# Kernel optimization log

Measured on AMD Instinct MI355X. Metric: run time of the kernel, lower is better.

Reference implementation:

```python
import jax, jax.numpy as jnp
import numpy as np

NUM_SAMPLES = 8192   # num_parallel_samples
HIDDEN = 512
EMB = 40             # embedding_dim(10) * freq_map['H'](4)
C_IN = 1
TIME_FEAT = 4
HIST_LEN = 336
PRED_LEN = 48
MIN_SCALE = 1e-5
SAMPLE_KEY_SEED = 42


def _gru_cell(h, x, W_ih, W_hh, b_ih, b_hh):
    # torch GRU cell: gates stacked as [r, z, n] along rows of W (each HIDDEN)
    gi = x @ W_ih.T + b_ih            # [B, 3H]
    gh = h @ W_hh.T + b_hh            # [B, 3H]
    H = h.shape[-1]
    i_r, i_z, i_n = gi[:, :H], gi[:, H:2 * H], gi[:, 2 * H:]
    h_r, h_z, h_n = gh[:, :H], gh[:, H:2 * H], gh[:, 2 * H:]
    r = jax.nn.sigmoid(i_r + h_r)
    z = jax.nn.sigmoid(i_z + h_z)
    n = jnp.tanh(i_n + r * h_n)
    return (1.0 - z) * n + z * h


def setup_inputs() -> dict:
    key = jax.random.key(0)
    ks = jax.random.split(key, 16)
    f32 = jnp.float32
    inp = {
        "x": jax.random.normal(ks[0], (1, HIST_LEN, C_IN), dtype=f32),
        "x_mark": jax.random.normal(ks[1], (1, HIST_LEN, TIME_FEAT), dtype=f32),
        "y_mark": jax.random.normal(ks[2], (1, PRED_LEN, TIME_FEAT), dtype=f32),
        "mode": 0,
        # time_feat_embedding: Linear(4 -> 40), torch layout [out, in]
        "W_emb": jax.random.normal(ks[3], (EMB, TIME_FEAT), dtype=f32) * 0.05,
        "b_emb": jnp.zeros((EMB,), dtype=f32),
        # GRU (1 layer): input size = c_in + EMB = 41
        "W_ih": jax.random.normal(ks[4], (3 * HIDDEN, C_IN + EMB), dtype=f32) * 0.05,
        "W_hh": jax.random.normal(ks[5], (3 * HIDDEN, HIDDEN), dtype=f32) * 0.05,
        "b_ih": jnp.zeros((3 * HIDDEN,), dtype=f32),
        "b_hh": jnp.zeros((3 * HIDDEN,), dtype=f32),
        # StudentT args projection: three Linear(HIDDEN -> 1)
        "W_df": jax.random.normal(ks[6], (1, HIDDEN), dtype=f32) * 0.05,
        "b_df": jnp.zeros((1,), dtype=f32),
        "W_loc": jax.random.normal(ks[7], (1, HIDDEN), dtype=f32) * 0.05,
        "b_loc": jnp.zeros((1,), dtype=f32),
        "W_sc": jax.random.normal(ks[8], (1, HIDDEN), dtype=f32) * 0.05,
        "b_sc": jnp.zeros((1,), dtype=f32),
    }
    return inp


def _deepar_sample(x, x_mark, y_mark, W_emb, b_emb, W_ih, W_hh, b_ih, b_hh,
                   W_df, b_df, W_loc, b_loc, W_sc, b_sc):
    S = NUM_SAMPLES
    # ---- encoder (unroll_encoder with y=None) ----
    scale = jnp.clip(jnp.mean(jnp.abs(x), axis=1, keepdims=True), MIN_SCALE, None)  # [1,1,1]
    seq = x / scale
    tfe = x_mark @ W_emb.T + b_emb                      # [1, T, EMB]
    enc_in = jnp.concatenate([seq, tfe], axis=-1)       # [1, T, 41]
    h0 = jnp.zeros((1, HIDDEN), dtype=x.dtype)

    def enc_step(h, xt):  # xt: [1, 41]
        h = _gru_cell(h, xt, W_ih, W_hh, b_ih, b_hh)
        return h, None

    h_T, _ = jax.lax.scan(enc_step, h0, jnp.swapaxes(enc_in, 0, 1))  # [1, H]

    # ---- sampling decoder ----
    h = jnp.broadcast_to(h_T, (S, HIDDEN))              # repeat state across samples
    # note: original feeds the UNSCALED last observation as first decoder input
    tgt0 = jnp.broadcast_to(x[0, -1, :], (S, C_IN))     # [S, 1]
    emb_y = y_mark[0] @ W_emb.T + b_emb                 # [pred_len, EMB]
    scale_s = scale[0, 0, 0]                            # scalar (batch=1, c=1)
    base_key = jax.random.key(SAMPLE_KEY_SEED)

    def dec_step(carry, xs):
        h, tgt = carry
        e_k, k = xs
        inp = jnp.concatenate([tgt, jnp.broadcast_to(e_k, (S, EMB))], axis=-1)  # [S, 41]
        h = _gru_cell(h, inp, W_ih, W_hh, b_ih, b_hh)
        # StudentTOutput domain map: df = 2 + softplus, loc raw, scale = softplus
        df = 2.0 + jax.nn.softplus(h @ W_df.T + b_df)   # [S, 1]
        loc = h @ W_loc.T + b_loc                       # [S, 1]
        sc = jax.nn.softplus(h @ W_sc.T + b_sc)         # [S, 1]
        eps = jax.random.t(jax.random.fold_in(base_key, k),
                           jax.lax.stop_gradient(df), df.shape, dtype=df.dtype)
        sample = (loc + sc * eps) * scale_s             # AffineTransformed(scale)
        return (h, sample), sample

    ks = jnp.arange(PRED_LEN)
    _, samples = jax.lax.scan(dec_step, (h, tgt0), (emb_y, ks))  # [pred_len, S, 1]
    return jnp.transpose(samples, (1, 0, 2))            # [S, pred_len, c_out]


def reference(x, x_mark, y_mark, mode, W_emb, b_emb, W_ih, W_hh, b_ih, b_hh,
              W_df, b_df, W_loc, b_loc, W_sc, b_sc):
    # mode=0 -> sampling/inference path (the kernel target)
    return _deepar_sample(x, x_mark, y_mark, W_emb, b_emb, W_ih, W_hh, b_ih, b_hh,
                          W_df, b_df, W_loc, b_loc, W_sc, b_sc)
```

## Files before the change

kernel.cpp:

```cpp
#include <hip/hip_runtime.h>
#include <cmath>


#define JAX_PARTITIONABLE 1

#define HIDDEN 512
#define EMB 40
#define HIST 336
#define PRED 48
#define S_N 8192
#define ENC_BLOCKS 48

#define HPLANE (8192 * 512)
#define WPLANE (1536 * 512)
#define INV4096 (1.0f / 4096.0f)

typedef __attribute__((ext_vector_type(8))) _Float16 half8;
typedef __attribute__((ext_vector_type(4))) float f32x4;

struct KeyPair { unsigned a, b; };

__device__ __forceinline__ unsigned rotl32_(unsigned v, unsigned s) {
  return (v << s) | (v >> (32u - s));
}

__device__ __forceinline__ KeyPair tf2x32(KeyPair k, unsigned x0, unsigned x1) {
  unsigned ks0 = k.a, ks1 = k.b, ks2 = ks0 ^ ks1 ^ 0x1BD11BDAu;
  x0 += ks0; x1 += ks1;
#define TF_R(r) { x0 += x1; x1 = rotl32_(x1, r); x1 ^= x0; }
  TF_R(13u) TF_R(15u) TF_R(26u) TF_R(6u)  x0 += ks1; x1 += ks2 + 1u;
  TF_R(17u) TF_R(29u) TF_R(16u) TF_R(24u) x0 += ks2; x1 += ks0 + 2u;
  TF_R(13u) TF_R(15u) TF_R(26u) TF_R(6u)  x0 += ks0; x1 += ks1 + 3u;
  TF_R(17u) TF_R(29u) TF_R(16u) TF_R(24u) x0 += ks1; x1 += ks2 + 4u;
  TF_R(13u) TF_R(15u) TF_R(26u) TF_R(6u)  x0 += ks2; x1 += ks0 + 5u;
#undef TF_R
  KeyPair r; r.a = x0; r.b = x1; return r;
}

__device__ __forceinline__ void split2_(KeyPair key, KeyPair& r0, KeyPair& r1) {
#if JAX_PARTITIONABLE
  r0 = tf2x32(key, 0u, 0u);
  r1 = tf2x32(key, 0u, 1u);
#else
  KeyPair p0 = tf2x32(key, 0u, 2u);
  KeyPair p1 = tf2x32(key, 1u, 3u);
  r0.a = p0.a; r0.b = p1.a;
  r1.a = p0.b; r1.b = p1.b;
#endif
}

__device__ __forceinline__ void split3_(KeyPair key, KeyPair& r0, KeyPair& r1, KeyPair& r2) {
#if JAX_PARTITIONABLE
  r0 = tf2x32(key, 0u, 0u);
  r1 = tf2x32(key, 0u, 1u);
  r2 = tf2x32(key, 0u, 2u);
#else
  KeyPair p0 = tf2x32(key, 0u, 3u);
  KeyPair p1 = tf2x32(key, 1u, 4u);
  KeyPair p2 = tf2x32(key, 2u, 5u);
  r0.a = p0.a; r0.b = p1.a;
  r1.a = p2.a; r1.b = p0.b;
  r2.a = p1.b; r2.b = p2.b;
#endif
}

__device__ __forceinline__ unsigned scalar_bits_(KeyPair key) {
#if JAX_PARTITIONABLE
  KeyPair p = tf2x32(key, 0u, 0u);
  return p.a ^ p.b;
#else
  return tf2x32(key, 0u, 0u).a;
#endif
}

__device__ __forceinline__ unsigned batch_bits_8192_(KeyPair key, int s) {
#if JAX_PARTITIONABLE
  KeyPair p = tf2x32(key, 0u, (unsigned)s);
  return p.a ^ p.b;
#else
  if (s < 4096) return tf2x32(key, (unsigned)s, (unsigned)(4096 + s)).a;
  return tf2x32(key, (unsigned)(s - 4096), (unsigned)s).b;
#endif
}

__device__ __forceinline__ KeyPair subkey_of_8192_(KeyPair key, int s) {
#if JAX_PARTITIONABLE
  return tf2x32(key, 0u, (unsigned)s);
#else
  KeyPair r;
  if (s < 4096) {
    r.a = tf2x32(key, (unsigned)(2 * s),     (unsigned)(8192 + 2 * s)).a;
    r.b = tf2x32(key, (unsigned)(2 * s + 1), (unsigned)(8192 + 2 * s + 1)).a;
  } else {
    int m = 2 * s - 8192;
    r.a = tf2x32(key, (unsigned)m,       (unsigned)(m + 8192)).b;
    r.b = tf2x32(key, (unsigned)(m + 1), (unsigned)(m + 1 + 8192)).b;
  }
  return r;
#endif
}

__device__ __forceinline__ float acc_logf_(float x) {
  return (float)log((double)x);
}
__device__ __forceinline__ float acc_expf_(float x) {
  return (float)exp((double)x);
}

__device__ __forceinline__ float bits_to_uniform01_(unsigned bits) {
  return __uint_as_float((bits >> 9) | 0x3F800000u) - 1.0f;
}

__device__ __forceinline__ float xla_log1pf_(float t) {
  #pragma clang fp contract(off)
  float small_ = (1.0f + (-0.5f) * t) * t;
  float large_ = acc_logf_(t + 1.0f);
  return (fabsf(t) < 1e-4f) ? small_ : large_;
}

__device__ float xla_erfinv_(float x) {
  #pragma clang fp contract(off)
  float w = -xla_log1pf_(-(x * x));
  float p;
  if (w < 5.0f) {
    float ww = w - 2.5f;
    p = 2.81022636e-08f;
    p = 3.43273939e-07f + p * ww;
    p = -3.5233877e-06f + p * ww;
    p = -4.39150654e-06f + p * ww;
    p = 0.00021858087f + p * ww;
    p = -0.00125372503f + p * ww;
    p = -0.00417768164f + p * ww;
    p = 0.246640727f + p * ww;
    p = 1.50140941f + p * ww;
  } else {
    float ww = sqrtf(w) - 3.0f;
    p = -0.000200214257f;
    p = 0.000100950558f + p * ww;
    p = 0.00134934322f + p * ww;
    p = -0.00367342844f + p * ww;
    p = 0.00573950773f + p * ww;
    p = -0.0076224613f + p * ww;
    p = 0.00943887047f + p * ww;
    p = 1.00167406f + p * ww;
    p = 2.83297682f + p * ww;
  }
  return p * x;
}

__device__ float bits_to_normal_(unsigned bits) {
  #pragma clang fp contract(off)
  const float lo = __uint_as_float(0xBF7FFFFFu);
  float f = bits_to_uniform01_(bits);
  float u = f * 2.0f + lo;
  u = fmaxf(lo, u);
  return __uint_as_float(0x3FB504F3u) * xla_erfinv_(u);
}

__device__ __forceinline__ float softplus_(float x) {
  #pragma clang fp contract(off)
  float amax = fmaxf(x, 0.0f);
  float e = acc_expf_(-fabsf(x));
  return amax + xla_log1pf_(e);
}

__device__ __forceinline__ float sigmoid_(float v) { return 1.0f / (1.0f + expf(-v)); }

__device__ __forceinline__ unsigned short f2h_(float f) {
  _Float16 h = (_Float16)f;
  return __builtin_bit_cast(unsigned short, h);
}
__device__ __forceinline__ float h2f_(unsigned short b) {
  return (float)__builtin_bit_cast(_Float16, b);
}

__device__ float gamma_sample_(KeyPair gkey, float alpha) {
  #pragma clang fp contract(off)
  const float third = 0.33333334f;
  float d = alpha - third;
  float c = third / sqrtf(d);
  KeyPair key, boost_sub;
  split2_(gkey, key, boost_sub);
  (void)boost_sub;
  float X = 0.0f, V = 1.0f, U = 2.0f;
  for (int guard = 0; guard < 1024; guard++) {
    float X2 = X * X;
    float sq = 1.0f - 0.0331f * (X2 * X2);
    bool cont = false;
    if (U >= sq) {
      float lhs = acc_logf_(U);
      float rhs = (X * 0.5f) + (d * ((1.0f - V) + acc_logf_(V)));
      cont = (lhs >= rhs);
    }
    if (!cont) break;
    KeyPair nkey, xkey, Ukey;
    split3_(key, nkey, xkey, Ukey);
    key = nkey;
    float x, v;
    KeyPair kk = xkey;
    do {
      KeyPair knew, sub;
      split2_(kk, knew, sub);
      kk = knew;
      x = bits_to_normal_(scalar_bits_(sub));
      v = 1.0f + x * c;
    } while (v <= 0.0f);
    X = x * x;
    V = (v * v) * v;
    U = bits_to_uniform01_(scalar_bits_(Ukey));
  }
  return d * V;
}

__device__ float sample_t_eps_(int k, int s, float df) {
  #pragma clang fp contract(off)
  KeyPair base; base.a = 0u; base.b = 42u;
  KeyPair tkey = tf2x32(base, 0u, (unsigned)k);
  KeyPair key_n, key_g;
  split2_(tkey, key_n, key_g);
  float n = bits_to_normal_(batch_bits_8192_(key_n, s));
  KeyPair gkey = subkey_of_8192_(key_g, s);
  float half_df = df * 0.5f;
  float g = gamma_sample_(gkey, half_df);
  return n * sqrtf(half_df / g);
}


__global__ __launch_bounds__(256) void prep_kernel(
    const float* __restrict__ x, const float* __restrict__ x_mark,
    const float* __restrict__ y_mark, const float* __restrict__ W_emb,
    const float* __restrict__ b_emb, float* __restrict__ scale_p,
    float* __restrict__ tfe, float* __restrict__ emb_y,
    unsigned* __restrict__ flags) {
  int tid = threadIdx.x;
  if (tid == 0) {
    float s = 0.0f;
    for (int t = 0; t < HIST; t++) s += fabsf(x[t]);
    float m = s / 336.0f;
    scale_p[0] = fmaxf(m, 1e-5f);
  }
  for (int i = tid; i < ENC_BLOCKS * 16; i += 256) flags[i] = 0u;
  for (int idx = tid; idx < HIST * EMB; idx += 256) {
    int t = idx / EMB, e = idx % EMB;
    float a = b_emb[e];
    for (int f = 0; f < 4; f++) a += x_mark[t * 4 + f] * W_emb[e * 4 + f];
    tfe[idx] = a;
  }
  for (int idx = tid; idx < PRED * EMB; idx += 256) {
    int kk = idx / EMB, e = idx % EMB;
    float a = b_emb[e];
    for (int f = 0; f < 4; f++) a += y_mark[kk * 4 + f] * W_emb[e * 4 + f];
    emb_y[idx] = a;
  }
}

__global__ __launch_bounds__(256) void enc_gi_kernel(
    const float* __restrict__ x, const float* __restrict__ tfe,
    const float* __restrict__ W_ih, const float* __restrict__ b_ih,
    const float* __restrict__ scale_p, float* __restrict__ enc_gi) {
  __shared__ float fe[EMB];
  __shared__ float xs_s;
  int t = blockIdx.x;
  int tid = threadIdx.x;
  if (tid < EMB) fe[tid] = tfe[t * EMB + tid];
  if (tid == 0) xs_s = x[t] / scale_p[0];
  __syncthreads();
  float xs = xs_s;
  for (int r = tid; r < 3 * HIDDEN; r += 256) {
    const float* wr = W_ih + (size_t)r * 41;
    float a = b_ih[r] + wr[0] * xs;
    #pragma unroll
    for (int e = 0; e < EMB; e++) a += wr[1 + e] * fe[e];
    enc_gi[(size_t)t * 1536 + r] = a;
  }
}

__global__ __launch_bounds__(256) void giy_kernel(
    const float* __restrict__ emb_y, const float* __restrict__ W_ih,
    const float* __restrict__ b_ih, float* __restrict__ giy) {
  __shared__ float fe[EMB];
  int k = blockIdx.x;
  int tid = threadIdx.x;
  if (tid < EMB) fe[tid] = emb_y[k * EMB + tid];
  __syncthreads();
  for (int r = tid; r < 3 * HIDDEN; r += 256) {
    const float* wr = W_ih + (size_t)r * 41;
    float a = b_ih[r];
    #pragma unroll
    for (int e = 0; e < EMB; e++) a += wr[1 + e] * fe[e];
    giy[(size_t)k * 1536 + r] = a;
  }
}

__global__ __launch_bounds__(256) void wsplit_kernel(
    const float* __restrict__ W_hh, unsigned short* __restrict__ Wr) {
  int row = blockIdx.x;
  int g = row >> 9;
  int jg = row & 511;
  int jb = jg >> 5, jl = jg & 31;
  size_t dst = ((size_t)jb * 96 + g * 32 + jl) * 512;
  for (int k = threadIdx.x; k < 512; k += 256) {
    float w = W_hh[(size_t)row * 512 + k];
    unsigned short g0 = f2h_(w);
    float r1 = (w - h2f_(g0)) * 4096.0f;
    unsigned short g1 = f2h_(r1);
    Wr[dst + k] = g0;
    Wr[WPLANE + dst + k] = g1;
  }
}

__global__ __launch_bounds__(256) void hsplit_kernel(
    const float* __restrict__ h_T, unsigned short* __restrict__ sT) {
  int i = threadIdx.x;
  for (int j = i; j < 512; j += 256) {
    float v = h_T[j];
    unsigned short f0 = f2h_(v);
    float r1 = (v - h2f_(f0)) * 4096.0f;
    sT[j] = f0;
    sT[512 + j] = f2h_(r1);
  }
}

__global__ __launch_bounds__(128) void h2bcast_kernel(
    const unsigned short* __restrict__ sT, unsigned short* __restrict__ h2) {
  int row = blockIdx.x;
  int tid = threadIdx.x;
  int sp = tid >> 6, c = tid & 63;
  ((uint4*)(h2 + (size_t)sp * HPLANE + (size_t)row * 512))[c] =
      ((const uint4*)(sT + sp * 512))[c];
}

__global__ __launch_bounds__(256) void enc_gru_kernel(
    const float* __restrict__ enc_gi, const float* __restrict__ W_hh,
    const float* __restrict__ b_hh, float* __restrict__ ghbuf,
    unsigned* __restrict__ flags, float* __restrict__ h_T) {
  __shared__ __align__(16) float hs[HIDDEN];
  int tid = threadIdx.x;
  int gtid = blockIdx.x * 256 + tid;
  int row = gtid >> 3;
  int sub = gtid & 7;

  float w[64];
  const float* wp = W_hh + (size_t)row * HIDDEN + sub * 64;
  #pragma unroll
  for (int i = 0; i < 16; i++) {
    float4 v = *(const float4*)(wp + 4 * i);
    w[4 * i + 0] = v.x; w[4 * i + 1] = v.y; w[4 * i + 2] = v.z; w[4 * i + 3] = v.w;
  }
  if (tid < 128) *(float4*)&hs[tid * 4] = make_float4(0.f, 0.f, 0.f, 0.f);
  float bhr0 = b_hh[tid],       bhz0 = b_hh[512 + tid],  bhn0 = b_hh[1024 + tid];
  float bhr1 = b_hh[256 + tid], bhz1 = b_hh[768 + tid],  bhn1 = b_hh[1280 + tid];
  __syncthreads();

  for (int t = 0; t < HIST; t++) {
    float p = 0.0f;
    const float4* hv = (const float4*)&hs[sub * 64];
    #pragma unroll
    for (int i = 0; i < 16; i++) {
      float4 v = hv[i];
      p += w[4 * i + 0] * v.x + w[4 * i + 1] * v.y +
           w[4 * i + 2] * v.z + w[4 * i + 3] * v.w;
    }
    p += __shfl_xor(p, 1, 64);
    p += __shfl_xor(p, 2, 64);
    p += __shfl_xor(p, 4, 64);
    int par = t & 1;
    if (sub == 0)
      __hip_atomic_store(&ghbuf[par * 1536 + row], p, __ATOMIC_RELAXED,
                         __HIP_MEMORY_SCOPE_AGENT);
    __syncthreads();
    if (tid == 0)
      __hip_atomic_store(&flags[blockIdx.x * 16], (unsigned)(t + 1),
                         __ATOMIC_RELEASE, __HIP_MEMORY_SCOPE_AGENT);
    if (tid < ENC_BLOCKS) {
      while (__hip_atomic_load(&flags[tid * 16], __ATOMIC_ACQUIRE,
                               __HIP_MEMORY_SCOPE_AGENT) < (unsigned)(t + 1))
        __builtin_amdgcn_s_sleep(1);
    }
    __syncthreads();
    float hn0, hn1;
    {
      int j = tid;
      float ghr = __hip_atomic_load(&ghbuf[par * 1536 + j], __ATOMIC_RELAXED, __HIP_MEMORY_SCOPE_AGENT);
      float ghz = __hip_atomic_load(&ghbuf[par * 1536 + 512 + j], __ATOMIC_RELAXED, __HIP_MEMORY_SCOPE_AGENT);
      float ghn = __hip_atomic_load(&ghbuf[par * 1536 + 1024 + j], __ATOMIC_RELAXED, __HIP_MEMORY_SCOPE_AGENT);
      float gir = enc_gi[(size_t)t * 1536 + j];
      float giz = enc_gi[(size_t)t * 1536 + 512 + j];
      float gin = enc_gi[(size_t)t * 1536 + 1024 + j];
      float r = sigmoid_(gir + (ghr + bhr0));
      float z = sigmoid_(giz + (ghz + bhz0));
      float n = tanhf(gin + r * (ghn + bhn0));
      hn0 = (1.0f - z) * n + z * hs[j];
    }
    {
      int j = tid + 256;
      float ghr = __hip_atomic_load(&ghbuf[par * 1536 + j], __ATOMIC_RELAXED, __HIP_MEMORY_SCOPE_AGENT);
      float ghz = __hip_atomic_load(&ghbuf[par * 1536 + 512 + j], __ATOMIC_RELAXED, __HIP_MEMORY_SCOPE_AGENT);
      float ghn = __hip_atomic_load(&ghbuf[par * 1536 + 1024 + j], __ATOMIC_RELAXED, __HIP_MEMORY_SCOPE_AGENT);
      float gir = enc_gi[(size_t)t * 1536 + j];
      float giz = enc_gi[(size_t)t * 1536 + 512 + j];
      float gin = enc_gi[(size_t)t * 1536 + 1024 + j];
      float r = sigmoid_(gir + (ghr + bhr1));
      float z = sigmoid_(giz + (ghz + bhz1));
      float n = tanhf(gin + r * (ghn + bhn1));
      hn1 = (1.0f - z) * n + z * hs[j];
    }
    hs[tid] = hn0;
    hs[tid + 256] = hn1;
    __syncthreads();
  }
  if (blockIdx.x == 0 && tid < 128)
    *(float4*)&h_T[tid * 4] = *(float4*)&hs[tid * 4];
}

__global__ __launch_bounds__(256, 2) void dec_gru_mfma(
    const unsigned short* __restrict__ h2_in,
    const unsigned short* __restrict__ Wr,
    const float* __restrict__ giy_k, const float* __restrict__ b_hh,
    const float* __restrict__ W_ih, const float* __restrict__ tgt,
    int tgt_is_x, unsigned short* __restrict__ h2_out,
    const float* __restrict__ W_df, const float* __restrict__ W_loc,
    const float* __restrict__ W_sc, float* __restrict__ partials) {
  __shared__ unsigned short As[2][2][128][32];
  int b_ = blockIdx.x;
  int xcd = b_ & 7, slot = b_ >> 3;
  int mb = xcd * 8 + (slot & 7);
  int jb = slot >> 3;
  int tid = threadIdx.x;
  int lane = tid & 63;
  int wave = tid >> 6;
  int wm = wave >> 1, wn = wave & 1;
  int s0 = mb * 128;
  int q = lane >> 4, c = lane & 15;

  f32x4 accm[4][3], accc[4][3];
  #pragma unroll
  for (int i = 0; i < 4; i++)
    #pragma unroll
    for (int g = 0; g < 3; g++) {
      accm[i][g] = (f32x4){0.f, 0.f, 0.f, 0.f};
      accc[i][g] = (f32x4){0.f, 0.f, 0.f, 0.f};
    }

  float hold[4][4];
  #pragma unroll
  for (int i = 0; i < 4; i++)
    #pragma unroll
    for (int r = 0; r < 4; r++) hold[i][r] = 0.f;

  int asp[4], arow[4], acol[4];
  #pragma unroll
  for (int r = 0; r < 4; r++) {
    int a = r * 256 + tid;
    asp[r] = a >> 9;
    int rem = a & 511;
    arow[r] = rem >> 2;
    acol[r] = rem & 3;
  }

  const unsigned short* Bbase =
      Wr + ((size_t)jb * 96 + wn * 16 + c) * 512 + q * 8;

  #pragma unroll
  for (int r = 0; r < 4; r++) {
    uint4 v = *(const uint4*)(h2_in + (size_t)asp[r] * HPLANE +
                              (size_t)(s0 + arow[r]) * 512 + acol[r] * 8);
    *(uint4*)&As[0][asp[r]][arow[r]][(acol[r] ^ (arow[r] & 3)) * 8] = v;
  }
  half8 Bcur[3][2];
  #pragma unroll
  for (int g = 0; g < 3; g++) {
    Bcur[g][0] = *(const half8*)(Bbase + (size_t)g * 32 * 512);
    Bcur[g][1] = *(const half8*)(Bbase + WPLANE + (size_t)g * 32 * 512);
  }
  __syncthreads();

  int cur = 0;
  for (int kbi = 0; kbi < 16; kbi++) {
    int kb = kbi * 32;
    uint4 Areg[4];
    half8 Bn[3][2];
    if (kbi < 15) {
      #pragma unroll
      for (int r = 0; r < 4; r++)
        Areg[r] = *(const uint4*)(h2_in + (size_t)asp[r] * HPLANE +
                                  (size_t)(s0 + arow[r]) * 512 + kb + 32 +
                                  acol[r] * 8);
      #pragma unroll
      for (int g = 0; g < 3; g++) {
        Bn[g][0] = *(const half8*)(Bbase + (size_t)g * 32 * 512 + kb + 32);
        Bn[g][1] = *(const half8*)(Bbase + WPLANE + (size_t)g * 32 * 512 + kb + 32);
      }
    }
    if (kbi == jb) {
      int cc = wn * 16 + c;
      #pragma unroll
      for (int i = 0; i < 4; i++)
        #pragma unroll
        for (int reg = 0; reg < 4; reg++) {
          int m = wm * 64 + i * 16 + q * 4 + reg;
          int idx = (((cc >> 3) ^ (m & 3)) << 3) + (cc & 7);
          hold[i][reg] = h2f_(As[cur][0][m][idx]) +
                         h2f_(As[cur][1][m][idx]) * INV4096;
        }
    }
    #pragma unroll
    for (int i = 0; i < 4; i++) {
      int m = wm * 64 + i * 16 + c;
      half8 a0 = *(const half8*)&As[cur][0][m][(q ^ (c & 3)) * 8];
      half8 a1 = *(const half8*)&As[cur][1][m][(q ^ (c & 3)) * 8];
      #pragma unroll
      for (int g = 0; g < 3; g++) {
        accm[i][g] = __builtin_amdgcn_mfma_f32_16x16x32_f16(a0, Bcur[g][0], accm[i][g], 0, 0, 0);
        accc[i][g] = __builtin_amdgcn_mfma_f32_16x16x32_f16(a0, Bcur[g][1], accc[i][g], 0, 0, 0);
        accc[i][g] = __builtin_amdgcn_mfma_f32_16x16x32_f16(a1, Bcur[g][0], accc[i][g], 0, 0, 0);
      }
    }
    if (kbi < 15) {
      #pragma unroll
      for (int r = 0; r < 4; r++)
        *(uint4*)&As[cur ^ 1][asp[r]][arow[r]][(acol[r] ^ (arow[r] & 3)) * 8] =
            Areg[r];
      #pragma unroll
      for (int g = 0; g < 3; g++) {
        Bcur[g][0] = Bn[g][0];
        Bcur[g][1] = Bn[g][1];
      }
    }
    __syncthreads();
    cur ^= 1;
  }

  float* pb = (float*)&As[0][0][0][0];
  {
    int j = jb * 32 + wn * 16 + c;
    float gyr = giy_k[j], gyz = giy_k[512 + j], gyn = giy_k[1024 + j];
    float w0r = W_ih[(size_t)j * 41];
    float w0z = W_ih[(size_t)(512 + j) * 41];
    float w0n = W_ih[(size_t)(1024 + j) * 41];
    float bhr = b_hh[j], bhz = b_hh[512 + j], bhn = b_hh[1024 + j];
    float wdj = W_df[j], wlj = W_loc[j], wsj = W_sc[j];
    #pragma unroll
    for (int i = 0; i < 4; i++) {
      #pragma unroll
      for (int reg = 0; reg < 4; reg++) {
        int s = s0 + wm * 64 + i * 16 + q * 4 + reg;
        float tg = tgt_is_x ? tgt[HIST - 1] : tgt[s];
        size_t off = (size_t)s * 512 + j;
        float h_old = hold[i][reg];
        float ghr = accm[i][0][reg] + accc[i][0][reg] * INV4096;
        float ghz = accm[i][1][reg] + accc[i][1][reg] * INV4096;
        float ghn = accm[i][2][reg] + accc[i][2][reg] * INV4096;
        float gr = (gyr + w0r * tg) + (ghr + bhr);
        float gz = (gyz + w0z * tg) + (ghz + bhz);
        float gn_i = gyn + w0n * tg;
        float gn_h = ghn + bhn;
        float r_ = sigmoid_(gr);
        float z_ = sigmoid_(gz);
        float n_ = tanhf(gn_i + r_ * gn_h);
        float hn = (1.0f - z_) * n_ + z_ * h_old;
        unsigned short f0 = f2h_(hn);
        float r1 = (hn - h2f_(f0)) * 4096.0f;
        __builtin_nontemporal_store(f0, &h2_out[off]);
        __builtin_nontemporal_store(f2h_(r1), &h2_out[HPLANE + off]);
        float vd = hn * wdj, vl = hn * wlj, vs = hn * wsj;
        #pragma unroll
        for (int o = 1; o < 16; o <<= 1) {
          vd += __shfl_xor(vd, o, 64);
          vl += __shfl_xor(vl, o, 64);
          vs += __shfl_xor(vs, o, 64);
        }
        if (c == 0) {
          int sl = i * 16 + q * 4 + reg;
          int bix = ((wm * 2 + wn) * 64 + sl) * 3;
          pb[bix + 0] = vd; pb[bix + 1] = vl; pb[bix + 2] = vs;
        }
      }
    }
  }
  __syncthreads();
  if (tid < 128) {
    int wmh = tid >> 6, sl = tid & 63;
    int ia = (wmh * 2 + 0) * 192 + sl * 3;
    int ib = ia + 192;
    int s = s0 + wmh * 64 + sl;
    size_t pofs = (size_t)s * 48 + jb * 3;
    partials[pofs + 0] = pb[ia + 0] + pb[ib + 0];
    partials[pofs + 1] = pb[ia + 1] + pb[ib + 1];
    partials[pofs + 2] = pb[ia + 2] + pb[ib + 2];
  }
}

__global__ __launch_bounds__(64) void dec_head_kernel(
    const float* __restrict__ partials, const float* __restrict__ b_df,
    const float* __restrict__ b_loc, const float* __restrict__ b_sc,
    const float* __restrict__ scale_p, float* __restrict__ tgt,
    float* __restrict__ out, int k) {
  #pragma clang fp contract(off)
  int s = blockIdx.x * 64 + threadIdx.x;
  const float* p = partials + (size_t)s * 48;
  float adf = 0.f, alo = 0.f, asc = 0.f;
  #pragma unroll
  for (int jb = 0; jb < 16; jb++) {
    adf += p[jb * 3 + 0];
    alo += p[jb * 3 + 1];
    asc += p[jb * 3 + 2];
  }
  float df = 2.0f + softplus_(adf + b_df[0]);
  float loc = alo + b_loc[0];
  float sc = softplus_(asc + b_sc[0]);
  float eps = sample_t_eps_(k, s, df);
  float smp = (loc + sc * eps) * scale_p[0];
  out[(size_t)s * PRED + k] = smp;
  tgt[s] = smp;
}

extern "C" void kernel_launch(void* const* d_in, const int* in_sizes, int n_in,
                              void* d_out, int out_size, void* d_ws, size_t ws_size,
                              hipStream_t stream) {
  const float* x      = (const float*)d_in[0];
  const float* x_mark = (const float*)d_in[1];
  const float* y_mark = (const float*)d_in[2];
  const float* W_emb  = (const float*)d_in[4];
  const float* b_emb  = (const float*)d_in[5];
  const float* W_ih   = (const float*)d_in[6];
  const float* W_hh   = (const float*)d_in[7];
  const float* b_ih   = (const float*)d_in[8];
  const float* b_hh   = (const float*)d_in[9];
  const float* W_df   = (const float*)d_in[10];
  const float* b_df   = (const float*)d_in[11];
  const float* W_loc  = (const float*)d_in[12];
  const float* b_loc  = (const float*)d_in[13];
  const float* W_sc   = (const float*)d_in[14];
  const float* b_sc   = (const float*)d_in[15];
  float* out = (float*)d_out;

  float* w = (float*)d_ws;
  unsigned short* h2_a = (unsigned short*)(w);
  unsigned short* h2_b = (unsigned short*)(w + 4194304);
  unsigned short* Wr   = (unsigned short*)(w + 8388608);
  float* enc_gi = w + 9175040;
  float* giy    = w + 9691136;
  float* tfe    = w + 9764864;
  float* emb_y  = w + 9778304;
  float* ghbuf  = w + 9780224;
  float* h_T    = w + 9783296;
  unsigned short* sT = (unsigned short*)(w + 9783808);
  float* tgt    = w + 9784320;
  float* scale_p = w + 9792512;
  unsigned* flags = (unsigned*)(w + 9792516);
  float* partials = w + 9793540;

  prep_kernel<<<1, 256, 0, stream>>>(x, x_mark, y_mark, W_emb, b_emb,
                                     scale_p, tfe, emb_y, flags);
  enc_gi_kernel<<<HIST, 256, 0, stream>>>(x, tfe, W_ih, b_ih, scale_p, enc_gi);
  giy_kernel<<<PRED, 256, 0, stream>>>(emb_y, W_ih, b_ih, giy);
  wsplit_kernel<<<1536, 256, 0, stream>>>(W_hh, Wr);
  enc_gru_kernel<<<ENC_BLOCKS, 256, 0, stream>>>(enc_gi, W_hh, b_hh, ghbuf,
                                                 flags, h_T);
  hsplit_kernel<<<1, 256, 0, stream>>>(h_T, sT);
  h2bcast_kernel<<<S_N, 128, 0, stream>>>(sT, h2_a);

  for (int k = 0; k < PRED; k++) {
    const unsigned short* h_in = (k % 2 == 0) ? h2_a : h2_b;
    unsigned short* h_o = (k % 2 == 0) ? h2_b : h2_a;
    dec_gru_mfma<<<1024, 256, 0, stream>>>(
        h_in, Wr, giy + (size_t)k * 1536, b_hh, W_ih,
        (k == 0) ? x : tgt, (k == 0) ? 1 : 0, h_o,
        W_df, W_loc, W_sc, partials);
    dec_head_kernel<<<S_N / 64, 64, 0, stream>>>(
        partials, b_df, b_loc, b_sc, scale_p, tgt, out, k);
  }
}
```

Baseline: 5.618 ms.

## Replace encoder flag barrier with tagged 64-bit values and double-buffered hidden state

The encoder GRU grid barrier (per-block release flags, an acquire spin by 48 threads, and two __syncthreads) is replaced by packing each gate dot-product with a step tag into a 64-bit word. Every thread spins directly on the six values it needs until their tags match. The hidden state in shared memory is double-buffered so one __syncthreads per step is enough, and the enc_gi loads are hoisted ahead of the dot product to hide their latency. The cost is more global polling traffic from all threads, and correctness relies on the 64-bit stores and loads being atomic.

```diff
diff --git a/kernel.cpp b/kernel.cpp
--- a/kernel.cpp
+++ b/kernel.cpp
@@ -231,7 +231,7 @@
     const float* __restrict__ y_mark, const float* __restrict__ W_emb,
     const float* __restrict__ b_emb, float* __restrict__ scale_p,
     float* __restrict__ tfe, float* __restrict__ emb_y,
-    unsigned* __restrict__ flags) {
+    unsigned long long* __restrict__ gh2) {
   int tid = threadIdx.x;
   if (tid == 0) {
     float s = 0.0f;
@@ -239,7 +239,7 @@
     float m = s / 336.0f;
     scale_p[0] = fmaxf(m, 1e-5f);
   }
-  for (int i = tid; i < ENC_BLOCKS * 16; i += 256) flags[i] = 0u;
+  for (int i = tid; i < 2 * 1536; i += 256) gh2[i] = 0ull;
   for (int idx = tid; idx < HIST * EMB; idx += 256) {
     int t = idx / EMB, e = idx % EMB;
     float a = b_emb[e];
@@ -332,9 +332,9 @@
 
 __global__ __launch_bounds__(256) void enc_gru_kernel(
     const float* __restrict__ enc_gi, const float* __restrict__ W_hh,
-    const float* __restrict__ b_hh, float* __restrict__ ghbuf,
-    unsigned* __restrict__ flags, float* __restrict__ h_T) {
-  __shared__ __align__(16) float hs[HIDDEN];
+    const float* __restrict__ b_hh, unsigned long long* __restrict__ gh2,
+    float* __restrict__ h_T) {
+  __shared__ __align__(16) float hsb[2][HIDDEN];
   int tid = threadIdx.x;
   int gtid = blockIdx.x * 256 + tid;
   int row = gtid >> 3;
@@ -347,14 +347,23 @@
     float4 v = *(const float4*)(wp + 4 * i);
     w[4 * i + 0] = v.x; w[4 * i + 1] = v.y; w[4 * i + 2] = v.z; w[4 * i + 3] = v.w;
   }
-  if (tid < 128) *(float4*)&hs[tid * 4] = make_float4(0.f, 0.f, 0.f, 0.f);
+  if (tid < 128) *(float4*)&hsb[0][tid * 4] = make_float4(0.f, 0.f, 0.f, 0.f);
   float bhr0 = b_hh[tid],       bhz0 = b_hh[512 + tid],  bhn0 = b_hh[1024 + tid];
   float bhr1 = b_hh[256 + tid], bhz1 = b_hh[768 + tid],  bhn1 = b_hh[1280 + tid];
   __syncthreads();
 
   for (int t = 0; t < HIST; t++) {
+    int par = t & 1;
+    unsigned tag = (unsigned)(t + 1);
+    const float* hc = hsb[par];
+    float* hw = hsb[par ^ 1];
+
+    const float* gi = enc_gi + (size_t)t * 1536;
+    float gir0 = gi[tid],        giz0 = gi[512 + tid],  gin0 = gi[1024 + tid];
+    float gir1 = gi[256 + tid],  giz1 = gi[768 + tid],  gin1 = gi[1280 + tid];
+
     float p = 0.0f;
-    const float4* hv = (const float4*)&hs[sub * 64];
+    const float4* hv = (const float4*)&hc[sub * 64];
     #pragma unroll
     for (int i = 0; i < 16; i++) {
       float4 v = hv[i];
@@ -364,53 +373,51 @@
     p += __shfl_xor(p, 1, 64);
     p += __shfl_xor(p, 2, 64);
     p += __shfl_xor(p, 4, 64);
-    int par = t & 1;
-    if (sub == 0)
-      __hip_atomic_store(&ghbuf[par * 1536 + row], p, __ATOMIC_RELAXED,
+    if (sub == 0) {
+      unsigned long long pk =
+          ((unsigned long long)tag << 32) | (unsigned long long)__float_as_uint(p);
+      __hip_atomic_store(&gh2[par * 1536 + row], pk, __ATOMIC_RELAXED,
                          __HIP_MEMORY_SCOPE_AGENT);
+    }
+
+    const unsigned long long* g = gh2 + par * 1536;
+    unsigned long long v0, v1, v2, v3, v4, v5;
+    for (;;) {
+      v0 = __hip_atomic_load(&g[tid],         __ATOMIC_RELAXED, __HIP_MEMORY_SCOPE_AGENT);
+      v1 = __hip_atomic_load(&g[512 + tid],   __ATOMIC_RELAXED, __HIP_MEMORY_SCOPE_AGENT);
+      v2 = __hip_atomic_load(&g[1024 + tid],  __ATOMIC_RELAXED, __HIP_MEMORY_SCOPE_AGENT);
+      v3 = __hip_atomic_load(&g[256 + tid],   __ATOMIC_RELAXED, __HIP_MEMORY_SCOPE_AGENT);
+      v4 = __hip_atomic_load(&g[768 + tid],   __ATOMIC_RELAXED, __HIP_MEMORY_SCOPE_AGENT);
+      v5 = __hip_atomic_load(&g[1280 + tid],  __ATOMIC_RELAXED, __HIP_MEMORY_SCOPE_AGENT);
+      if ((unsigned)(v0 >> 32) == tag && (unsigned)(v1 >> 32) == tag &&
+          (unsigned)(v2 >> 32) == tag && (unsigned)(v3 >> 32) == tag &&
+          (unsigned)(v4 >> 32) == tag && (unsigned)(v5 >> 32) == tag)
+        break;
+      __builtin_amdgcn_s_sleep(1);
+    }
+
+    {
+      float ghr = __uint_as_float((unsigned)v0);
+      float ghz = __uint_as_float((unsigned)v1);
+      float ghn = __uint_as_float((unsigned)v2);
+      float r = sigmoid_(gir0 + (ghr + bhr0));
+      float z = sigmoid_(giz0 + (ghz + bhz0));
+      float n = tanhf(gin0 + r * (ghn + bhn0));
+      hw[tid] = (1.0f - z) * n + z * hc[tid];
+    }
+    {
+      float ghr = __uint_as_float((unsigned)v3);
+      float ghz = __uint_as_float((unsigned)v4);
+      float ghn = __uint_as_float((unsigned)v5);
+      float r = sigmoid_(gir1 + (ghr + bhr1));
+      float z = sigmoid_(giz1 + (ghz + bhz1));
+      float n = tanhf(gin1 + r * (ghn + bhn1));
+      hw[tid + 256] = (1.0f - z) * n + z * hc[tid + 256];
+    }
     __syncthreads();
-    if (tid == 0)
-      __hip_atomic_store(&flags[blockIdx.x * 16], (unsigned)(t + 1),
-                         __ATOMIC_RELEASE, __HIP_MEMORY_SCOPE_AGENT);
-    if (tid < ENC_BLOCKS) {
-      while (__hip_atomic_load(&flags[tid * 16], __ATOMIC_ACQUIRE,
-                               __HIP_MEMORY_SCOPE_AGENT) < (unsigned)(t + 1))
-        __builtin_amdgcn_s_sleep(1);
-    }
-    __syncthreads();
-    float hn0, hn1;
-    {
-      int j = tid;
-      float ghr = __hip_atomic_load(&ghbuf[par * 1536 + j], __ATOMIC_RELAXED, __HIP_MEMORY_SCOPE_AGENT);
-      float ghz = __hip_atomic_load(&ghbuf[par * 1536 + 512 + j], __ATOMIC_RELAXED, __HIP_MEMORY_SCOPE_AGENT);
-      float ghn = __hip_atomic_load(&ghbuf[par * 1536 + 1024 + j], __ATOMIC_RELAXED, __HIP_MEMORY_SCOPE_AGENT);
-      float gir = enc_gi[(size_t)t * 1536 + j];
-      float giz = enc_gi[(size_t)t * 1536 + 512 + j];
-      float gin = enc_gi[(size_t)t * 1536 + 1024 + j];
-      float r = sigmoid_(gir + (ghr + bhr0));
-      float z = sigmoid_(giz + (ghz + bhz0));
-      float n = tanhf(gin + r * (ghn + bhn0));
-      hn0 = (1.0f - z) * n + z * hs[j];
-    }
-    {
-      int j = tid + 256;
-      float ghr = __hip_atomic_load(&ghbuf[par * 1536 + j], __ATOMIC_RELAXED, __HIP_MEMORY_SCOPE_AGENT);
-      float ghz = __hip_atomic_load(&ghbuf[par * 1536 + 512 + j], __ATOMIC_RELAXED, __HIP_MEMORY_SCOPE_AGENT);
-      float ghn = __hip_atomic_load(&ghbuf[par * 1536 + 1024 + j], __ATOMIC_RELAXED, __HIP_MEMORY_SCOPE_AGENT);
-      float gir = enc_gi[(size_t)t * 1536 + j];
-      float giz = enc_gi[(size_t)t * 1536 + 512 + j];
-      float gin = enc_gi[(size_t)t * 1536 + 1024 + j];
-      float r = sigmoid_(gir + (ghr + bhr1));
-      float z = sigmoid_(giz + (ghz + bhz1));
-      float n = tanhf(gin + r * (ghn + bhn1));
-      hn1 = (1.0f - z) * n + z * hs[j];
-    }
-    hs[tid] = hn0;
-    hs[tid + 256] = hn1;
-    __syncthreads();
   }
   if (blockIdx.x == 0 && tid < 128)
-    *(float4*)&h_T[tid * 4] = *(float4*)&hs[tid * 4];
+    *(float4*)&h_T[tid * 4] = *(float4*)&hsb[0][tid * 4];
 }
 
 __global__ __launch_bounds__(256, 2) void dec_gru_mfma(
@@ -643,21 +650,19 @@
   float* giy    = w + 9691136;
   float* tfe    = w + 9764864;
   float* emb_y  = w + 9778304;
-  float* ghbuf  = w + 9780224;
-  float* h_T    = w + 9783296;
-  unsigned short* sT = (unsigned short*)(w + 9783808);
-  float* tgt    = w + 9784320;
-  float* scale_p = w + 9792512;
-  unsigned* flags = (unsigned*)(w + 9792516);
-  float* partials = w + 9793540;
+  unsigned long long* gh2 = (unsigned long long*)(w + 9780224);
+  float* h_T    = w + 9786368;
+  unsigned short* sT = (unsigned short*)(w + 9786880);
+  float* tgt    = w + 9787392;
+  float* scale_p = w + 9795584;
+  float* partials = w + 9795588;
 
   prep_kernel<<<1, 256, 0, stream>>>(x, x_mark, y_mark, W_emb, b_emb,
-                                     scale_p, tfe, emb_y, flags);
+                                     scale_p, tfe, emb_y, gh2);
   enc_gi_kernel<<<HIST, 256, 0, stream>>>(x, tfe, W_ih, b_ih, scale_p, enc_gi);
   giy_kernel<<<PRED, 256, 0, stream>>>(emb_y, W_ih, b_ih, giy);
   wsplit_kernel<<<1536, 256, 0, stream>>>(W_hh, Wr);
-  enc_gru_kernel<<<ENC_BLOCKS, 256, 0, stream>>>(enc_gi, W_hh, b_hh, ghbuf,
-                                                 flags, h_T);
+  enc_gru_kernel<<<ENC_BLOCKS, 256, 0, stream>>>(enc_gi, W_hh, b_hh, gh2, h_T);
   hsplit_kernel<<<1, 256, 0, stream>>>(h_T, sT);
   h2bcast_kernel<<<S_N, 128, 0, stream>>>(sT, h2_a);
 
```

Measured after the change: 5.258 ms. 6.4% less time.
